# Kernel tuning notes

Hardware: AMD Instinct MI355X
Metric: run time of the kernel (lower is better)

## Reference

```python
import jax, jax.numpy as jnp
import numpy as np

ALPHA = 8.3  # depth similarity sharpness, F_D = exp(-alpha*|D(p0)-D(pn)|) (depth-aware CNN)
PAD, STRIDE, DIL, KH, KW = 1, 1, 1, 3, 3


def setup_inputs() -> dict:
    key = jax.random.key(0)
    k1, k2, k3, k4 = jax.random.split(key, 4)
    B, C_in, C_out, H, W = 2, 32, 32, 512, 512
    x = jax.random.normal(k1, (B, C_in, H, W), dtype=jnp.float32)
    depth = jax.random.uniform(k2, (B, 1, H, W), dtype=jnp.float32)
    weight = jax.random.normal(k3, (C_out, C_in, KH, KW), dtype=jnp.float32) * 0.05
    bias = jax.random.normal(k4, (C_out,), dtype=jnp.float32) * 0.05
    return {"x": x, "depth": depth, "weight": weight, "bias": bias}


def _depthconv(x, depth, weight, bias):
    B, C, H, W = x.shape
    C_out = weight.shape[0]
    H_out = (H + 2 * PAD - DIL * (KH - 1) - 1) // STRIDE + 1
    W_out = (W + 2 * PAD - DIL * (KW - 1) - 1) // STRIDE + 1
    x_p = jnp.pad(x, ((0, 0), (0, 0), (PAD, PAD), (PAD, PAD)))
    d_p = jnp.pad(depth, ((0, 0), (0, 0), (PAD, PAD), (PAD, PAD)))
    # depth at the receptive-field center of each output pixel, [B,1,H_out,W_out]
    ci, cj = (KH // 2) * DIL, (KW // 2) * DIL
    d_c = d_p[:, :, ci:ci + H_out * STRIDE:STRIDE, cj:cj + W_out * STRIDE:STRIDE]
    out = jnp.broadcast_to(bias[None, :, None, None], (B, C_out, H_out, W_out)).astype(x.dtype)
    for ki in range(KH):
        for kj in range(KW):
            hs, ws = ki * DIL, kj * DIL
            xs = x_p[:, :, hs:hs + H_out * STRIDE:STRIDE, ws:ws + W_out * STRIDE:STRIDE]
            ds = d_p[:, :, hs:hs + H_out * STRIDE:STRIDE, ws:ws + W_out * STRIDE:STRIDE]
            sim = jnp.exp(-ALPHA * jnp.abs(d_c - ds))  # [B,1,H_out,W_out]
            out = out + jnp.einsum('oc,bchw->bohw', weight[:, :, ki, kj], xs * sim)
    return out


def reference(x, depth, weight, bias):
    return _depthconv(x, depth, weight, bias)
```

## Files before the change

kernel.cpp:

```cpp
#include <hip/hip_runtime.h>

typedef _Float16 half8 __attribute__((ext_vector_type(8)));
typedef float floatx4 __attribute__((ext_vector_type(4)));

constexpr int C = 32, H = 512, W = 512, HW = H * W;
constexpr int TBH = 8;
constexpr int TBW = 32;
constexpr int RR  = TBH + 2;
constexpr int PX  = TBW + 8;
constexpr int PXW = 20;
constexpr int ROWW = PX * PXW + 4;

__device__ __forceinline__ unsigned pack2h(float lo, float hi) {
    unsigned a = (unsigned)__builtin_bit_cast(unsigned short, (_Float16)lo);
    unsigned b = (unsigned)__builtin_bit_cast(unsigned short, (_Float16)hi);
    return a | (b << 16);
}

__global__ __launch_bounds__(256) void pack_w(const float* __restrict__ weight,
                                              uint4* __restrict__ wp) {
    int j = blockIdx.x * 256 + threadIdx.x;
    if (j >= 1152) return;
    int lane = j & 63, half = (j >> 6) & 1, tap = j >> 7;
    int o = half * 16 + (lane & 15), q = lane >> 4;
    uint4 v;
    v.x = pack2h(weight[(o * 32 + q * 8 + 0) * 9 + tap], weight[(o * 32 + q * 8 + 1) * 9 + tap]);
    v.y = pack2h(weight[(o * 32 + q * 8 + 2) * 9 + tap], weight[(o * 32 + q * 8 + 3) * 9 + tap]);
    v.z = pack2h(weight[(o * 32 + q * 8 + 4) * 9 + tap], weight[(o * 32 + q * 8 + 5) * 9 + tap]);
    v.w = pack2h(weight[(o * 32 + q * 8 + 6) * 9 + tap], weight[(o * 32 + q * 8 + 7) * 9 + tap]);
    wp[j] = v;
}

__global__ __launch_bounds__(256, 4) void depthconv_fused(
    const float* __restrict__ x, const float* __restrict__ depth,
    const uint4* __restrict__ wp, const float* __restrict__ bias,
    float* __restrict__ out)
{
    __shared__ __attribute__((aligned(16))) unsigned xsl[RR * ROWW];

    const int bid  = blockIdx.x;
    const int wseg = bid & 15, hseg = (bid >> 4) & 63, b = bid >> 10;
    const int h0 = hseg * TBH, w0 = wseg * TBW;
    const int tid = threadIdx.x;

    const int lane = tid & 63, wid = tid >> 6;
    const int nn = lane & 15, q = lane >> 4;
    const int chh = wid >> 1;
    const int pcl = (wid & 1) * 16 + nn;

    half8 af[9];
    #pragma unroll
    for (int tap = 0; tap < 9; ++tap)
        af[tap] = __builtin_bit_cast(half8, wp[(tap * 2 + chh) * 64 + lane]);

    floatx4 acc[TBH];
    #pragma unroll
    for (int i = 0; i < 4; ++i) {
        float bv = bias[chh * 16 + q * 4 + i];
        #pragma unroll
        for (int o = 0; o < TBH; ++o) acc[o][i] = bv;
    }

    #pragma unroll
    for (int k = 0; k < 7; ++k) {
        int u = tid + k * 256;
        if (u < 16 * RR * (PX / 4)) {
            int f4 = u % 10, t = u / 10;
            int r = t % RR, cp = t / RR;
            int h = h0 - 1 + r, wst = w0 - 4 + f4 * 4;
            bool valid = ((unsigned)h < (unsigned)H) && ((unsigned)wst < (unsigned)W);
            float4 va = {0.f, 0.f, 0.f, 0.f}, vb = {0.f, 0.f, 0.f, 0.f};
            if (valid) {
                const float* xb = x + ((size_t)(b * C + 2 * cp)) * HW + (size_t)h * W + wst;
                va = *(const float4*)xb;
                vb = *(const float4*)(xb + HW);
            }
            unsigned* dst = &xsl[r * ROWW + (f4 * 4) * PXW + cp];
            dst[0 * PXW] = pack2h(va.x, vb.x);
            dst[1 * PXW] = pack2h(va.y, vb.y);
            dst[2 * PXW] = pack2h(va.z, vb.z);
            dst[3 * PXW] = pack2h(va.w, vb.w);
        }
    }

    #pragma unroll
    for (int k = 0; k < 2; ++k) {
        int u = tid + k * 256;
        if (u < RR * PX) {
            int px = u % PX, r = u / PX;
            int h = h0 - 1 + r, ww = w0 - 4 + px;
            bool valid = ((unsigned)h < (unsigned)H) && ((unsigned)ww < (unsigned)W);
            float d = valid ? depth[(size_t)b * HW + (size_t)h * W + ww] : 0.f;
            float2 e = valid ? make_float2(__expf(-8.3f * d), __expf(8.3f * d))
                             : make_float2(0.f, 0.f);
            *(float2*)&xsl[r * ROWW + px * PXW + 16] = e;
        }
    }

    __syncthreads();

    float2 dc[TBH];
    #pragma unroll
    for (int o = 0; o < TBH; ++o)
        dc[o] = *(const float2*)&xsl[(o + 1) * ROWW + (pcl + 4) * PXW + 16];

    #pragma unroll
    for (int r = 0; r < RR; ++r) {
        uint4 xraw[3]; float2 dn[3];
        #pragma unroll
        for (int kj = 0; kj < 3; ++kj) {
            int p = pcl + 3 + kj;
            xraw[kj] = *(const uint4*)&xsl[r * ROWW + p * PXW + 4 * q];
            dn[kj]   = *(const float2*)&xsl[r * ROWW + p * PXW + 16];
        }
        #pragma unroll
        for (int kj = 0; kj < 3; ++kj) {
            #pragma unroll
            for (int ki = 0; ki < 3; ++ki) {
                int o = r - ki;
                if (o < 0 || o >= TBH) continue;
                int tap = ki * 3 + kj;
                float s = fminf(dn[kj].y * dc[o].x, dn[kj].x * dc[o].y);
                _Float16 hs = (_Float16)s;
                half8 sv = { hs, hs, hs, hs, hs, hs, hs, hs };
                half8 bf = __builtin_bit_cast(half8, xraw[kj]) * sv;
                acc[o] = __builtin_amdgcn_mfma_f32_16x16x32_f16(af[tap], bf, acc[o], 0, 0, 0);
            }
        }
    }

    const int pw = w0 + pcl;
    #pragma unroll
    for (int o = 0; o < TBH; ++o) {
        float* op = out + (size_t)b * C * HW + (size_t)(h0 + o) * W + pw;
        #pragma unroll
        for (int i = 0; i < 4; ++i)
            op[(size_t)(chh * 16 + q * 4 + i) * HW] = acc[o][i];
    }
}

extern "C" void kernel_launch(void* const* d_in, const int* in_sizes, int n_in,
                              void* d_out, int out_size, void* d_ws, size_t ws_size,
                              hipStream_t stream) {
    const float* x      = (const float*)d_in[0];
    const float* depth  = (const float*)d_in[1];
    const float* weight = (const float*)d_in[2];
    const float* bias   = (const float*)d_in[3];
    float* out          = (float*)d_out;

    uint4* wpk = (uint4*)d_ws;

    hipLaunchKernelGGL(pack_w, dim3(5), dim3(256), 0, stream, weight, wpk);
    hipLaunchKernelGGL(depthconv_fused, dim3(2 * 64 * 16), dim3(256), 0, stream,
                       x, depth, wpk, bias, out);
}
```

Measured before the change: 142.5 us.

## Process two row tiles per block with register-prefetched second halo

Each block now computes 16 output rows as two 8-row sub-tiles sharing an 18-row LDS buffer. The extra 8 input rows and their depth values are loaded into registers before the first compute phase and written to LDS after it. This reuses the halo rows between the sub-tiles and overlaps global loads with MFMA work. Block-to-tile mapping is also remapped so adjacent width segments land on the same XCD. The costs are higher register and LDS use (launch bounds lowered to 2 blocks per SM) and half as many blocks.

```diff
diff --git a/kernel.cpp b/kernel.cpp
--- a/kernel.cpp
+++ b/kernel.cpp
@@ -4,12 +4,13 @@
 typedef float floatx4 __attribute__((ext_vector_type(4)));
 
 constexpr int C = 32, H = 512, W = 512, HW = H * W;
-constexpr int TBH = 8;
 constexpr int TBW = 32;
-constexpr int RR  = TBH + 2;
+constexpr int TLH = 8;
+constexpr int NT  = 2;
 constexpr int PX  = TBW + 8;
 constexpr int PXW = 20;
 constexpr int ROWW = PX * PXW + 4;
+constexpr int NSLOT = 18;
 
 __device__ __forceinline__ unsigned pack2h(float lo, float hi) {
     unsigned a = (unsigned)__builtin_bit_cast(unsigned short, (_Float16)lo);
@@ -31,16 +32,18 @@
     wp[j] = v;
 }
 
-__global__ __launch_bounds__(256, 4) void depthconv_fused(
+__global__ __launch_bounds__(256, 2) void depthconv_fused(
     const float* __restrict__ x, const float* __restrict__ depth,
     const uint4* __restrict__ wp, const float* __restrict__ bias,
     float* __restrict__ out)
 {
-    __shared__ __attribute__((aligned(16))) unsigned xsl[RR * ROWW];
+    __shared__ __attribute__((aligned(16))) unsigned xsl[NSLOT * ROWW];
 
     const int bid  = blockIdx.x;
-    const int wseg = bid & 15, hseg = (bid >> 4) & 63, b = bid >> 10;
-    const int h0 = hseg * TBH, w0 = wseg * TBW;
+    const int xcd  = bid & 7, sub = (bid >> 3) & 1;
+    const int hseg = (bid >> 4) & 31, b = bid >> 9;
+    const int wseg = xcd * 2 + sub;
+    const int h0 = hseg * (TLH * NT), w0 = wseg * TBW;
     const int tid = threadIdx.x;
 
     const int lane = tid & 63, wid = tid >> 6;
@@ -52,21 +55,15 @@
     #pragma unroll
     for (int tap = 0; tap < 9; ++tap)
         af[tap] = __builtin_bit_cast(half8, wp[(tap * 2 + chh) * 64 + lane]);
-
-    floatx4 acc[TBH];
-    #pragma unroll
-    for (int i = 0; i < 4; ++i) {
-        float bv = bias[chh * 16 + q * 4 + i];
-        #pragma unroll
-        for (int o = 0; o < TBH; ++o) acc[o][i] = bv;
-    }
+    float bv[4];
+    #pragma unroll
+    for (int i = 0; i < 4; ++i) bv[i] = bias[chh * 16 + q * 4 + i];
 
     #pragma unroll
     for (int k = 0; k < 7; ++k) {
         int u = tid + k * 256;
-        if (u < 16 * RR * (PX / 4)) {
-            int f4 = u % 10, t = u / 10;
-            int r = t % RR, cp = t / RR;
+        if (u < 1600) {
+            int f4 = u % 10, t = u / 10, r = t % 10, cp = t / 10;
             int h = h0 - 1 + r, wst = w0 - 4 + f4 * 4;
             bool valid = ((unsigned)h < (unsigned)H) && ((unsigned)wst < (unsigned)W);
             float4 va = {0.f, 0.f, 0.f, 0.f}, vb = {0.f, 0.f, 0.f, 0.f};
@@ -83,10 +80,23 @@
         }
     }
 
+    float4 hva[5], hvb[5];
+    #pragma unroll
+    for (int uu = 0; uu < 5; ++uu) {
+        int u = tid + uu * 256;
+        int f4 = u % 10, t = u / 10, r = t & 7, cp = t >> 3;
+        int h = h0 + 9 + r, wst = w0 - 4 + f4 * 4;
+        bool valid = ((unsigned)h < (unsigned)H) && ((unsigned)wst < (unsigned)W);
+        float4 z = {0.f, 0.f, 0.f, 0.f};
+        const float* xb = x + ((size_t)(b * C + 2 * cp)) * HW + (size_t)h * W + wst;
+        hva[uu] = valid ? *(const float4*)xb : z;
+        hvb[uu] = valid ? *(const float4*)(xb + HW) : z;
+    }
+
     #pragma unroll
     for (int k = 0; k < 2; ++k) {
         int u = tid + k * 256;
-        if (u < RR * PX) {
+        if (u < 400) {
             int px = u % PX, r = u / PX;
             int h = h0 - 1 + r, ww = w0 - 4 + px;
             bool valid = ((unsigned)h < (unsigned)H) && ((unsigned)ww < (unsigned)W);
@@ -97,45 +107,102 @@
         }
     }
 
+    float hd0 = 0.f, hd1 = 0.f;
+    {
+        int px = tid % PX, r = tid / PX;
+        int h = h0 + 9 + r, ww = w0 - 4 + px;
+        if (((unsigned)h < (unsigned)H) && ((unsigned)ww < (unsigned)W))
+            hd0 = depth[(size_t)b * HW + (size_t)h * W + ww];
+    }
+    if (tid < 64) {
+        int u = tid + 256; int px = u % PX, r = u / PX;
+        int h = h0 + 9 + r, ww = w0 - 4 + px;
+        if (((unsigned)h < (unsigned)H) && ((unsigned)ww < (unsigned)W))
+            hd1 = depth[(size_t)b * HW + (size_t)h * W + ww];
+    }
+
     __syncthreads();
 
-    float2 dc[TBH];
-    #pragma unroll
-    for (int o = 0; o < TBH; ++o)
-        dc[o] = *(const float2*)&xsl[(o + 1) * ROWW + (pcl + 4) * PXW + 16];
-
-    #pragma unroll
-    for (int r = 0; r < RR; ++r) {
-        uint4 xraw[3]; float2 dn[3];
-        #pragma unroll
-        for (int kj = 0; kj < 3; ++kj) {
-            int p = pcl + 3 + kj;
-            xraw[kj] = *(const uint4*)&xsl[r * ROWW + p * PXW + 4 * q];
-            dn[kj]   = *(const float2*)&xsl[r * ROWW + p * PXW + 16];
-        }
-        #pragma unroll
-        for (int kj = 0; kj < 3; ++kj) {
-            #pragma unroll
-            for (int ki = 0; ki < 3; ++ki) {
-                int o = r - ki;
-                if (o < 0 || o >= TBH) continue;
-                int tap = ki * 3 + kj;
-                float s = fminf(dn[kj].y * dc[o].x, dn[kj].x * dc[o].y);
-                _Float16 hs = (_Float16)s;
-                half8 sv = { hs, hs, hs, hs, hs, hs, hs, hs };
-                half8 bf = __builtin_bit_cast(half8, xraw[kj]) * sv;
-                acc[o] = __builtin_amdgcn_mfma_f32_16x16x32_f16(af[tap], bf, acc[o], 0, 0, 0);
-            }
-        }
-    }
-
-    const int pw = w0 + pcl;
-    #pragma unroll
-    for (int o = 0; o < TBH; ++o) {
-        float* op = out + (size_t)b * C * HW + (size_t)(h0 + o) * W + pw;
-        #pragma unroll
-        for (int i = 0; i < 4; ++i)
-            op[(size_t)(chh * 16 + q * 4 + i) * HW] = acc[o][i];
+    #pragma unroll
+    for (int kt = 0; kt < NT; ++kt) {
+        floatx4 acc[TLH];
+        #pragma unroll
+        for (int i = 0; i < 4; ++i) {
+            float bvv = bv[i];
+            #pragma unroll
+            for (int o = 0; o < TLH; ++o) acc[o][i] = bvv;
+        }
+
+        float2 dc[TLH];
+        #pragma unroll
+        for (int o = 0; o < TLH; ++o)
+            dc[o] = *(const float2*)&xsl[(kt * 8 + o + 1) * ROWW + (pcl + 4) * PXW + 16];
+
+        #pragma unroll
+        for (int r = 0; r < 10; ++r) {
+            const int slot = kt * 8 + r;
+            uint4 xraw[3]; float2 dn[3];
+            #pragma unroll
+            for (int kj = 0; kj < 3; ++kj) {
+                int p = pcl + 3 + kj;
+                xraw[kj] = *(const uint4*)&xsl[slot * ROWW + p * PXW + 4 * q];
+                dn[kj]   = *(const float2*)&xsl[slot * ROWW + p * PXW + 16];
+            }
+            #pragma unroll
+            for (int kj = 0; kj < 3; ++kj) {
+                #pragma unroll
+                for (int ki = 0; ki < 3; ++ki) {
+                    int o = r - ki;
+                    if (o < 0 || o >= TLH) continue;
+                    int tap = ki * 3 + kj;
+                    float s = fminf(dn[kj].y * dc[o].x, dn[kj].x * dc[o].y);
+                    _Float16 hs = (_Float16)s;
+                    half8 sv = { hs, hs, hs, hs, hs, hs, hs, hs };
+                    half8 bf = __builtin_bit_cast(half8, xraw[kj]) * sv;
+                    acc[o] = __builtin_amdgcn_mfma_f32_16x16x32_f16(af[tap], bf, acc[o], 0, 0, 0);
+                }
+            }
+        }
+
+        const int pw = w0 + pcl;
+        #pragma unroll
+        for (int o = 0; o < TLH; ++o) {
+            float* op = out + (size_t)b * C * HW + (size_t)(h0 + kt * 8 + o) * W + pw;
+            #pragma unroll
+            for (int i = 0; i < 4; ++i)
+                op[(size_t)(chh * 16 + q * 4 + i) * HW] = acc[o][i];
+        }
+
+        if (kt + 1 < NT) {
+            #pragma unroll
+            for (int uu = 0; uu < 5; ++uu) {
+                int u = tid + uu * 256;
+                int f4 = u % 10, t = u / 10, r = t & 7, cp = t >> 3;
+                unsigned* dst = &xsl[(10 + r) * ROWW + (f4 * 4) * PXW + cp];
+                float4 va = hva[uu], vb = hvb[uu];
+                dst[0 * PXW] = pack2h(va.x, vb.x);
+                dst[1 * PXW] = pack2h(va.y, vb.y);
+                dst[2 * PXW] = pack2h(va.z, vb.z);
+                dst[3 * PXW] = pack2h(va.w, vb.w);
+            }
+            {
+                int px = tid % PX, r = tid / PX;
+                int h = h0 + 9 + r, ww = w0 - 4 + px;
+                bool valid = ((unsigned)h < (unsigned)H) && ((unsigned)ww < (unsigned)W);
+                float2 e = valid ? make_float2(__expf(-8.3f * hd0), __expf(8.3f * hd0))
+                                 : make_float2(0.f, 0.f);
+                *(float2*)&xsl[(10 + r) * ROWW + px * PXW + 16] = e;
+            }
+            if (tid < 64) {
+                int u = tid + 256; int px = u % PX, r = u / PX;
+                int h = h0 + 9 + r, ww = w0 - 4 + px;
+                bool valid = ((unsigned)h < (unsigned)H) && ((unsigned)ww < (unsigned)W);
+                float2 e = valid ? make_float2(__expf(-8.3f * hd1), __expf(8.3f * hd1))
+                                 : make_float2(0.f, 0.f);
+                *(float2*)&xsl[(10 + r) * ROWW + px * PXW + 16] = e;
+            }
+            __syncthreads();
+        }
     }
 }
 
@@ -151,6 +218,6 @@
     uint4* wpk = (uint4*)d_ws;
 
     hipLaunchKernelGGL(pack_w, dim3(5), dim3(256), 0, stream, weight, wpk);
-    hipLaunchKernelGGL(depthconv_fused, dim3(2 * 64 * 16), dim3(256), 0, stream,
+    hipLaunchKernelGGL(depthconv_fused, dim3(1024), dim3(256), 0, stream,
                        x, depth, wpk, bias, out);
 }
```

Result: no change. 144.8 us (+1.6%).

## Switch to 32x32x16 MFMA with per-wave output rows and swizzled LDS

Applied to the files above, without the earlier changes.

Replaces the 16x16x32 MFMA scheme with 32x32x16 MFMAs, where each wave computes one output row across all 32 output channels and 32 pixels. It splits the K dimension across two accumulators. Weights are now read from global/L1 inside the loop instead of held in registers. The tile height drops from 8 to 4, doubling the grid, and block indices are remapped to spread width segments across XCDs. An XOR swizzle is added to the LDS channel layout to cut bank conflicts. This lowers register pressure and halo reuse per block, at the cost of more halo loads and repeated weight fetches.

```diff
diff --git a/kernel.cpp b/kernel.cpp
--- a/kernel.cpp
+++ b/kernel.cpp
@@ -1,11 +1,11 @@
 #include <hip/hip_runtime.h>
 
 typedef _Float16 half8 __attribute__((ext_vector_type(8)));
-typedef float floatx4 __attribute__((ext_vector_type(4)));
+typedef float floatx16 __attribute__((ext_vector_type(16)));
 
 constexpr int C = 32, H = 512, W = 512, HW = H * W;
-constexpr int TBH = 8;
 constexpr int TBW = 32;
+constexpr int TBH = 4;
 constexpr int RR  = TBH + 2;
 constexpr int PX  = TBW + 8;
 constexpr int PXW = 20;
@@ -21,13 +21,14 @@
                                               uint4* __restrict__ wp) {
     int j = blockIdx.x * 256 + threadIdx.x;
     if (j >= 1152) return;
-    int lane = j & 63, half = (j >> 6) & 1, tap = j >> 7;
-    int o = half * 16 + (lane & 15), q = lane >> 4;
+    int lane = j & 63, kh = (j >> 6) & 1, tap = j >> 7;
+    int m = lane & 31, hh = lane >> 5;
+    const float* wb = weight + (size_t)(m * 32 + kh * 16 + hh * 8) * 9 + tap;
     uint4 v;
-    v.x = pack2h(weight[(o * 32 + q * 8 + 0) * 9 + tap], weight[(o * 32 + q * 8 + 1) * 9 + tap]);
-    v.y = pack2h(weight[(o * 32 + q * 8 + 2) * 9 + tap], weight[(o * 32 + q * 8 + 3) * 9 + tap]);
-    v.z = pack2h(weight[(o * 32 + q * 8 + 4) * 9 + tap], weight[(o * 32 + q * 8 + 5) * 9 + tap]);
-    v.w = pack2h(weight[(o * 32 + q * 8 + 6) * 9 + tap], weight[(o * 32 + q * 8 + 7) * 9 + tap]);
+    v.x = pack2h(wb[0 * 9], wb[1 * 9]);
+    v.y = pack2h(wb[2 * 9], wb[3 * 9]);
+    v.z = pack2h(wb[4 * 9], wb[5 * 9]);
+    v.w = pack2h(wb[6 * 9], wb[7 * 9]);
     wp[j] = v;
 }
 
@@ -39,35 +40,19 @@
     __shared__ __attribute__((aligned(16))) unsigned xsl[RR * ROWW];
 
     const int bid  = blockIdx.x;
-    const int wseg = bid & 15, hseg = (bid >> 4) & 63, b = bid >> 10;
-    const int h0 = hseg * TBH, w0 = wseg * TBW;
+    const int xcd  = bid & 7, sub = (bid >> 3) & 1;
+    const int hseg = (bid >> 4) & 127, b = bid >> 11;
+    const int w0 = (xcd * 2 + sub) * TBW, h0 = hseg * TBH;
     const int tid = threadIdx.x;
-
     const int lane = tid & 63, wid = tid >> 6;
-    const int nn = lane & 15, q = lane >> 4;
-    const int chh = wid >> 1;
-    const int pcl = (wid & 1) * 16 + nn;
-
-    half8 af[9];
-    #pragma unroll
-    for (int tap = 0; tap < 9; ++tap)
-        af[tap] = __builtin_bit_cast(half8, wp[(tap * 2 + chh) * 64 + lane]);
-
-    floatx4 acc[TBH];
-    #pragma unroll
-    for (int i = 0; i < 4; ++i) {
-        float bv = bias[chh * 16 + q * 4 + i];
-        #pragma unroll
-        for (int o = 0; o < TBH; ++o) acc[o][i] = bv;
-    }
+    const int pcl = lane & 31, hh = lane >> 5;
 
     #pragma unroll
-    for (int k = 0; k < 7; ++k) {
+    for (int k = 0; k < 4; ++k) {
         int u = tid + k * 256;
-        if (u < 16 * RR * (PX / 4)) {
-            int f4 = u % 10, t = u / 10;
-            int r = t % RR, cp = t / RR;
-            int h = h0 - 1 + r, wst = w0 - 4 + f4 * 4;
+        if (u < 960) {
+            int f4 = u % 10, t = u / 10, cp = t & 15, r = t >> 4;
+            int h = h0 - 1 + r, wst = w0 - 4 + 4 * f4;
             bool valid = ((unsigned)h < (unsigned)H) && ((unsigned)wst < (unsigned)W);
             float4 va = {0.f, 0.f, 0.f, 0.f}, vb = {0.f, 0.f, 0.f, 0.f};
             if (valid) {
@@ -75,7 +60,8 @@
                 va = *(const float4*)xb;
                 vb = *(const float4*)(xb + HW);
             }
-            unsigned* dst = &xsl[r * ROWW + (f4 * 4) * PXW + cp];
+            int word = 4 * ((cp >> 2) ^ ((f4 >> 1) & 3)) + (cp & 3);
+            unsigned* dst = &xsl[r * ROWW + (4 * f4) * PXW + word];
             dst[0 * PXW] = pack2h(va.x, vb.x);
             dst[1 * PXW] = pack2h(va.y, vb.y);
             dst[2 * PXW] = pack2h(va.z, vb.z);
@@ -83,59 +69,59 @@
         }
     }
 
+    if (tid < RR * PX) {
+        int px = tid % PX, r = tid / PX;
+        int h = h0 - 1 + r, ww = w0 - 4 + px;
+        bool valid = ((unsigned)h < (unsigned)H) && ((unsigned)ww < (unsigned)W);
+        float d = valid ? depth[(size_t)b * HW + (size_t)h * W + ww] : 0.f;
+        float2 e = valid ? make_float2(__expf(-8.3f * d), __expf(8.3f * d))
+                         : make_float2(0.f, 0.f);
+        *(float2*)&xsl[r * ROWW + px * PXW + 16] = e;
+    }
+
+    floatx16 accA, accB;
     #pragma unroll
-    for (int k = 0; k < 2; ++k) {
-        int u = tid + k * 256;
-        if (u < RR * PX) {
-            int px = u % PX, r = u / PX;
-            int h = h0 - 1 + r, ww = w0 - 4 + px;
-            bool valid = ((unsigned)h < (unsigned)H) && ((unsigned)ww < (unsigned)W);
-            float d = valid ? depth[(size_t)b * HW + (size_t)h * W + ww] : 0.f;
-            float2 e = valid ? make_float2(__expf(-8.3f * d), __expf(8.3f * d))
-                             : make_float2(0.f, 0.f);
-            *(float2*)&xsl[r * ROWW + px * PXW + 16] = e;
-        }
+    for (int g = 0; g < 4; ++g) {
+        float4 bv = *(const float4*)(bias + g * 8 + 4 * hh);
+        accA[4 * g + 0] = bv.x; accA[4 * g + 1] = bv.y;
+        accA[4 * g + 2] = bv.z; accA[4 * g + 3] = bv.w;
+        accB[4 * g + 0] = 0.f;  accB[4 * g + 1] = 0.f;
+        accB[4 * g + 2] = 0.f;  accB[4 * g + 3] = 0.f;
     }
 
     __syncthreads();
 
-    float2 dc[TBH];
-    #pragma unroll
-    for (int o = 0; o < TBH; ++o)
-        dc[o] = *(const float2*)&xsl[(o + 1) * ROWW + (pcl + 4) * PXW + 16];
+    const float2 dc = *(const float2*)&xsl[(wid + 1) * ROWW + (pcl + 4) * PXW + 16];
 
     #pragma unroll
-    for (int r = 0; r < RR; ++r) {
-        uint4 xraw[3]; float2 dn[3];
-        #pragma unroll
+    for (int ki = 0; ki < 3; ++ki) {
+        const unsigned* srow = &xsl[(wid + ki) * ROWW];
+        const uint4* wpt = wp + (size_t)(ki * 3) * 128;
+        #pragma clang loop unroll(disable)
         for (int kj = 0; kj < 3; ++kj) {
             int p = pcl + 3 + kj;
-            xraw[kj] = *(const uint4*)&xsl[r * ROWW + p * PXW + 4 * q];
-            dn[kj]   = *(const float2*)&xsl[r * ROWW + p * PXW + 16];
-        }
-        #pragma unroll
-        for (int kj = 0; kj < 3; ++kj) {
-            #pragma unroll
-            for (int ki = 0; ki < 3; ++ki) {
-                int o = r - ki;
-                if (o < 0 || o >= TBH) continue;
-                int tap = ki * 3 + kj;
-                float s = fminf(dn[kj].y * dc[o].x, dn[kj].x * dc[o].y);
-                _Float16 hs = (_Float16)s;
-                half8 sv = { hs, hs, hs, hs, hs, hs, hs, hs };
-                half8 bf = __builtin_bit_cast(half8, xraw[kj]) * sv;
-                acc[o] = __builtin_amdgcn_mfma_f32_16x16x32_f16(af[tap], bf, acc[o], 0, 0, 0);
-            }
+            int key = (p >> 3) & 3;
+            const unsigned* rec = srow + p * PXW;
+            uint4 x0 = *(const uint4*)(rec + 4 * (hh ^ key));
+            uint4 x1 = *(const uint4*)(rec + 4 * ((2 + hh) ^ key));
+            float2 dn = *(const float2*)(rec + 16);
+            float s = fminf(dn.y * dc.x, dn.x * dc.y);
+            _Float16 hs = (_Float16)s;
+            half8 sv = { hs, hs, hs, hs, hs, hs, hs, hs };
+            half8 a0 = __builtin_bit_cast(half8, wpt[kj * 128 + lane]);
+            half8 a1 = __builtin_bit_cast(half8, wpt[kj * 128 + 64 + lane]);
+            accA = __builtin_amdgcn_mfma_f32_32x32x16_f16(
+                       a0, __builtin_bit_cast(half8, x0) * sv, accA, 0, 0, 0);
+            accB = __builtin_amdgcn_mfma_f32_32x32x16_f16(
+                       a1, __builtin_bit_cast(half8, x1) * sv, accB, 0, 0, 0);
         }
     }
 
-    const int pw = w0 + pcl;
+    float* op = out + (size_t)b * C * HW + (size_t)(h0 + wid) * W + w0 + pcl;
     #pragma unroll
-    for (int o = 0; o < TBH; ++o) {
-        float* op = out + (size_t)b * C * HW + (size_t)(h0 + o) * W + pw;
-        #pragma unroll
-        for (int i = 0; i < 4; ++i)
-            op[(size_t)(chh * 16 + q * 4 + i) * HW] = acc[o][i];
+    for (int i = 0; i < 16; ++i) {
+        int ch = (i & 3) + 8 * (i >> 2) + 4 * hh;
+        op[(size_t)ch * HW] = accA[i] + accB[i];
     }
 }
 
@@ -151,6 +137,6 @@
     uint4* wpk = (uint4*)d_ws;
 
     hipLaunchKernelGGL(pack_w, dim3(5), dim3(256), 0, stream, weight, wpk);
-    hipLaunchKernelGGL(depthconv_fused, dim3(2 * 64 * 16), dim3(256), 0, stream,
+    hipLaunchKernelGGL(depthconv_fused, dim3(4096), dim3(256), 0, stream,
                        x, depth, wpk, bias, out);
 }
```

Measured after the change: 144.9 us. Within noise of the previous version (+1.7%).
